# Kernel optimization log

Hardware: AMD Instinct MI355X
Metric: run time of the kernel (lower is better)

The kernel has to match this reference:

```python
import jax, jax.numpy as jnp
import numpy as np

N_M, N_D, N_A = 100000, 30000, 80000


def setup_inputs() -> dict:
    key = jax.random.key(0)
    ks = jax.random.split(key, 24)
    d_in, d_h, d_out = 64, 64, 32
    inp = {
        "x_movie": jax.random.normal(ks[0], (N_M, d_in), jnp.float32),
        "x_director": jax.random.normal(ks[1], (N_D, d_in), jnp.float32),
        "x_actor": jax.random.normal(ks[2], (N_A, d_in), jnp.float32),
        "src_md": jax.random.randint(ks[3], (1500000,), 0, N_M, jnp.int32),
        "dst_md": jax.random.randint(ks[4], (1500000,), 0, N_D, jnp.int32),
        "ew_md": jax.random.uniform(ks[5], (1500000,), jnp.float32),
        "src_dm": jax.random.randint(ks[6], (1500000,), 0, N_D, jnp.int32),
        "dst_dm": jax.random.randint(ks[7], (1500000,), 0, N_M, jnp.int32),
        "ew_dm": jax.random.uniform(ks[8], (1500000,), jnp.float32),
        "src_ma": jax.random.randint(ks[9], (2000000,), 0, N_M, jnp.int32),
        "dst_ma": jax.random.randint(ks[10], (2000000,), 0, N_A, jnp.int32),
        "ew_ma": jax.random.uniform(ks[11], (2000000,), jnp.float32),
        "src_am": jax.random.randint(ks[12], (2000000,), 0, N_A, jnp.int32),
        "dst_am": jax.random.randint(ks[13], (2000000,), 0, N_M, jnp.int32),
        "ew_am": jax.random.uniform(ks[14], (2000000,), jnp.float32),
        "W1_rel": jax.random.normal(ks[15], (4, d_in, d_h), jnp.float32) * 0.05,
        "b1": jax.random.normal(ks[16], (4, d_h), jnp.float32) * 0.05,
        "W1_root": jax.random.normal(ks[17], (4, d_in, d_h), jnp.float32) * 0.05,
        "W2_rel": jax.random.normal(ks[18], (4, d_h, d_out), jnp.float32) * 0.05,
        "b2": jax.random.normal(ks[19], (4, d_out), jnp.float32) * 0.05,
        "W2_root": jax.random.normal(ks[20], (4, d_h, d_out), jnp.float32) * 0.05,
    }
    return inp


def _hetero_layer(x_m, x_d, x_a, edges, ews, W_rel, b, W_root):
    # relation order: 0 = movie->director, 1 = director->movie,
    #                 2 = movie->actor,    3 = actor->movie
    (src_md, dst_md, src_dm, dst_dm, src_ma, dst_ma, src_am, dst_am) = edges
    (ew_md, ew_dm, ew_ma, ew_am) = ews
    # GraphConv: aggregate edge-weighted source features, then linear.
    agg_md = jax.ops.segment_sum(x_m[src_md] * ew_md[:, None], dst_md, num_segments=N_D)
    agg_dm = jax.ops.segment_sum(x_d[src_dm] * ew_dm[:, None], dst_dm, num_segments=N_M)
    agg_ma = jax.ops.segment_sum(x_m[src_ma] * ew_ma[:, None], dst_ma, num_segments=N_A)
    agg_am = jax.ops.segment_sum(x_a[src_am] * ew_am[:, None], dst_am, num_segments=N_M)
    out_d = agg_md @ W_rel[0] + b[0] + x_d @ W_root[0]
    out_m = (agg_dm @ W_rel[1] + b[1] + x_m @ W_root[1]) \
          + (agg_am @ W_rel[3] + b[3] + x_m @ W_root[3])  # HeteroConv aggr='sum'
    out_a = agg_ma @ W_rel[2] + b[2] + x_a @ W_root[2]
    return out_m, out_d, out_a


def reference(x_movie, x_director, x_actor,
              src_md, dst_md, ew_md, src_dm, dst_dm, ew_dm,
              src_ma, dst_ma, ew_ma, src_am, dst_am, ew_am,
              W1_rel, b1, W1_root, W2_rel, b2, W2_root):
    edges = (src_md, dst_md, src_dm, dst_dm, src_ma, dst_ma, src_am, dst_am)
    ews = (ew_md, ew_dm, ew_ma, ew_am)
    h_m, h_d, h_a = _hetero_layer(x_movie, x_director, x_actor, edges, ews, W1_rel, b1, W1_root)
    h_m, h_d, h_a = jax.nn.relu(h_m), jax.nn.relu(h_d), jax.nn.relu(h_a)
    o_m, o_d, o_a = _hetero_layer(h_m, h_d, h_a, edges, ews, W2_rel, b2, W2_root)
    return o_m, o_d, o_a
```

## Files before the change

### kernel.cpp

```cpp
#include <hip/hip_runtime.h>

#define N_M 100000
#define N_D 30000
#define N_A 80000

#define CSHIFT 14
#define NC_M 7
#define NC_D 2
#define NC_A 5

#define BO_MD 0
#define BO_DM (BO_MD + N_D * NC_M)
#define BO_MA (BO_DM + N_M * NC_D)
#define BO_AM (BO_MA + N_A * NC_M)
#define B_TOT (BO_AM + N_M * NC_A)

#define FBITS 12
#define NFINE 4096
#define NBUCK ((B_TOT + NFINE - 1) / NFINE)
#define T_A 4096

typedef unsigned int u32;
typedef unsigned short u16;
typedef unsigned long long u64;

__device__ __forceinline__ u16 f2bf(float f) {
  u32 u = __float_as_uint(f);
  return (u16)((u + 0x7FFFu + ((u >> 16) & 1u)) >> 16);
}
__device__ __forceinline__ float bf2f(u16 b) {
  return __uint_as_float(((u32)b) << 16);
}
__device__ __forceinline__ float bf2f_hi(u32 v) {
  return __uint_as_float(v & 0xFFFF0000u);
}
__device__ __forceinline__ u32 pack_edge(int src, float ew) {
  return ((u32)src << 15) | ((u32)f2bf(ew) & 0x7FFFu);
}
__device__ __forceinline__ float edge_w(u32 p) {
  return __uint_as_float((p & 0x7FFFu) << 16);
}

struct Rel { const int* src; const int* dst; const float* ew; int nE; int binBase; int nC; };
struct Rel4 { Rel r[4]; int blkStart[5]; };

__global__ __launch_bounds__(256) void phase0(Rel4 P, int* __restrict__ bucketHist) {
  __shared__ u32 lh[512];
  int tid = threadIdx.x;
  int b = blockIdx.x, s = 0;
  while (b >= P.blkStart[s + 1]) s++;
  const Rel R = P.r[s];
  int base = (b - P.blkStart[s]) * T_A;
  for (int i = tid; i < 512; i += 256) lh[i] = 0;
  __syncthreads();
#pragma unroll 4
  for (int k = 0; k < 16; k++) {
    int e = base + tid + k * 256;
    if (e < R.nE) {
      int key = R.binBase + R.dst[e] * R.nC + (R.src[e] >> CSHIFT);
      atomicAdd(&lh[key >> FBITS], 1u);
    }
  }
  __syncthreads();
  for (int i = tid; i < 512; i += 256) if (lh[i]) atomicAdd(&bucketHist[i], (int)lh[i]);
}

__global__ __launch_bounds__(256) void scan_bucket(const int* __restrict__ bucketHist,
                                                   int* __restrict__ bucketBase,
                                                   int* __restrict__ cursor) {
  __shared__ int wsum[4];
  int tid = threadIdx.x;
  int j0 = tid * 2;
  int a0 = (j0 < NBUCK) ? bucketHist[j0] : 0;
  int a1 = (j0 + 1 < NBUCK) ? bucketHist[j0 + 1] : 0;
  int ssum = a0 + a1;
  int lane = tid & 63, wid = tid >> 6;
  int sc = ssum;
#pragma unroll
  for (int off = 1; off < 64; off <<= 1) { int t = __shfl_up(sc, off, 64); if (lane >= off) sc += t; }
  if (lane == 63) wsum[wid] = sc;
  __syncthreads();
  int wex = 0, tot = 0;
  for (int w = 0; w < 4; w++) { int t = wsum[w]; if (w < wid) wex += t; tot += t; }
  int ex = wex + sc - ssum;
  if (j0 < NBUCK) { bucketBase[j0] = ex; cursor[j0] = ex; }
  if (j0 + 1 < NBUCK) { bucketBase[j0 + 1] = ex + a0; cursor[j0 + 1] = ex + a0; }
  if (tid == 0) bucketBase[NBUCK] = tot;
}

__global__ __launch_bounds__(256) void phaseA(Rel4 P, int* __restrict__ cursor,
                                              u64* __restrict__ tmp) {
  __shared__ u32 hist[512], lstart[512], cur[512], gbase[512];
  __shared__ u64 stage[T_A];
  __shared__ u32 wsum[4];
  int tid = threadIdx.x;
  int b = blockIdx.x, s = 0;
  while (b >= P.blkStart[s + 1]) s++;
  const Rel R = P.r[s];
  int base = (b - P.blkStart[s]) * T_A;
  int valid = min(T_A, R.nE - base);
  for (int i = tid; i < 512; i += 256) hist[i] = 0;
  __syncthreads();
#pragma unroll 4
  for (int k = 0; k < 16; k++) {
    int e = base + tid + k * 256;
    if (e < R.nE) {
      int key = R.binBase + R.dst[e] * R.nC + (R.src[e] >> CSHIFT);
      atomicAdd(&hist[key >> FBITS], 1u);
    }
  }
  __syncthreads();
  int c0 = tid * 2;
  u32 h0 = hist[c0], h1 = hist[c0 + 1];
  u32 ssum = h0 + h1;
  int lane = tid & 63, wid = tid >> 6;
  u32 sc = ssum;
#pragma unroll
  for (int off = 1; off < 64; off <<= 1) { int t = __shfl_up((int)sc, off, 64); if (lane >= off) sc += (u32)t; }
  if (lane == 63) wsum[wid] = sc;
  __syncthreads();
  u32 wex = 0;
  for (int w = 0; w < 4; w++) if (w < wid) wex += wsum[w];
  u32 ex = wex + sc - ssum;
// ... 58 lines not shown
  }
  if (c == NBUCK - 1 && tid == 0) bins[B_TOT] = s1;
  __syncthreads();
  for (int e = s0 + tid; e < s1; e += 256) {
    u64 t = tmp[e];
    u32 fine = (u32)(t >> 32) & (NFINE - 1);
    u32 pos = atomicAdd(&cur2[fine], 1u);
    pairs[s0 + pos] = (u32)t;
  }
}

__global__ __launch_bounds__(256) void l1_tr_m(
    const float* __restrict__ x,
    const float* __restrict__ Wr0, const float* __restrict__ Wr2,
    const float* __restrict__ Wt1, const float* __restrict__ Wt3,
    const float* __restrict__ b1a, const float* __restrict__ b1b,
    u16* __restrict__ t0, u16* __restrict__ t2, u16* __restrict__ r, int n) {
  __shared__ float A[4096], B[4096], C[4096];
  for (int i = threadIdx.x * 4; i < 4096; i += 1024) {
    *(float4*)&A[i] = *(const float4*)&Wr0[i];
    *(float4*)&B[i] = *(const float4*)&Wr2[i];
    float4 p = *(const float4*)&Wt1[i], q = *(const float4*)&Wt3[i];
    *(float4*)&C[i] = make_float4(p.x + q.x, p.y + q.y, p.z + q.z, p.w + q.w);
  }
  __syncthreads();
  int lane = threadIdx.x & 63, wid = threadIdx.x >> 6;
  int wave = blockIdx.x * 4 + wid, nW = gridDim.x * 4;
  float bj = b1a[lane] + b1b[lane];
  for (int base = wave * 4; base < n; base += nW * 4) {
    int n0 = base, n1 = min(base + 1, n - 1), n2 = min(base + 2, n - 1), n3 = min(base + 3, n - 1);
    float o0a = 0, o0b = 0, o0c = bj, o1a = 0, o1b = 0, o1c = bj;
    float o2a = 0, o2b = 0, o2c = bj, o3a = 0, o3b = 0, o3c = bj;
#pragma unroll 4
    for (int k = 0; k < 64; k++) {
      float wa = A[k * 64 + lane], wb = B[k * 64 + lane], wc = C[k * 64 + lane];
      float x0 = x[(size_t)n0 * 64 + k], x1 = x[(size_t)n1 * 64 + k];
      float x2 = x[(size_t)n2 * 64 + k], x3 = x[(size_t)n3 * 64 + k];
      o0a = fmaf(x0, wa, o0a); o0b = fmaf(x0, wb, o0b); o0c = fmaf(x0, wc, o0c);
      o1a = fmaf(x1, wa, o1a); o1b = fmaf(x1, wb, o1b); o1c = fmaf(x1, wc, o1c);
      o2a = fmaf(x2, wa, o2a); o2b = fmaf(x2, wb, o2b); o2c = fmaf(x2, wc, o2c);
      o3a = fmaf(x3, wa, o3a); o3b = fmaf(x3, wb, o3b); o3c = fmaf(x3, wc, o3c);
    }
    t0[(size_t)n0 * 64 + lane] = f2bf(o0a); t2[(size_t)n0 * 64 + lane] = f2bf(o0b); r[(size_t)n0 * 64 + lane] = f2bf(o0c);
    if (base + 1 < n) { t0[(size_t)n1 * 64 + lane] = f2bf(o1a); t2[(size_t)n1 * 64 + lane] = f2bf(o1b); r[(size_t)n1 * 64 + lane] = f2bf(o1c); }
    if (base + 2 < n) { t0[(size_t)n2 * 64 + lane] = f2bf(o2a); t2[(size_t)n2 * 64 + lane] = f2bf(o2b); r[(size_t)n2 * 64 + lane] = f2bf(o2c); }
    if (base + 3 < n) { t0[(size_t)n3 * 64 + lane] = f2bf(o3a); t2[(size_t)n3 * 64 + lane] = f2bf(o3b); r[(size_t)n3 * 64 + lane] = f2bf(o3c); }
  }
}

__global__ __launch_bounds__(256) void l1_tr_s(
    const float* __restrict__ x,
    const float* __restrict__ Wrel, const float* __restrict__ Wroot,
    const float* __restrict__ bias,
    u16* __restrict__ t, u16* __restrict__ r, int n) {
  __shared__ float A[4096], C[4096];
  for (int i = threadIdx.x * 4; i < 4096; i += 1024) {
    *(float4*)&A[i] = *(const float4*)&Wrel[i];
    *(float4*)&C[i] = *(const float4*)&Wroot[i];
  }
  __syncthreads();
  int lane = threadIdx.x & 63, wid = threadIdx.x >> 6;
  int wave = blockIdx.x * 4 + wid, nW = gridDim.x * 4;
  float bj = bias[lane];
  for (int base = wave * 4; base < n; base += nW * 4) {
    int n0 = base, n1 = min(base + 1, n - 1), n2 = min(base + 2, n - 1), n3 = min(base + 3, n - 1);
    float o0a = 0, o0c = bj, o1a = 0, o1c = bj, o2a = 0, o2c = bj, o3a = 0, o3c = bj;
#pragma unroll 4
    for (int k = 0; k < 64; k++) {
      float wa = A[k * 64 + lane], wc = C[k * 64 + lane];
      float x0 = x[(size_t)n0 * 64 + k], x1 = x[(size_t)n1 * 64 + k];
      float x2 = x[(size_t)n2 * 64 + k], x3 = x[(size_t)n3 * 64 + k];
      o0a = fmaf(x0, wa, o0a); o0c = fmaf(x0, wc, o0c);
      o1a = fmaf(x1, wa, o1a); o1c = fmaf(x1, wc, o1c);
      o2a = fmaf(x2, wa, o2a); o2c = fmaf(x2, wc, o2c);
      o3a = fmaf(x3, wa, o3a); o3c = fmaf(x3, wc, o3c);
    }
    t[(size_t)n0 * 64 + lane] = f2bf(o0a); r[(size_t)n0 * 64 + lane] = f2bf(o0c);
    if (base + 1 < n) { t[(size_t)n1 * 64 + lane] = f2bf(o1a); r[(size_t)n1 * 64 + lane] = f2bf(o1c); }
    if (base + 2 < n) { t[(size_t)n2 * 64 + lane] = f2bf(o2a); r[(size_t)n2 * 64 + lane] = f2bf(o2c); }
    if (base + 3 < n) { t[(size_t)n3 * 64 + lane] = f2bf(o3a); r[(size_t)n3 * 64 + lane] = f2bf(o3c); }
  }
}

__device__ __forceinline__ void gather2_seg64(
    int s0, int s1, const u32* __restrict__ pairs,
    const u16* __restrict__ tbl, int lanebyte, int half, int lane,
    float& a0, float& a1) {
  for (int base = s0; base < s1; base += 64) {
    int cnt = s1 - base; if (cnt > 64) cnt = 64;
    u32 pw = 0;
    if (base + lane < s1) pw = pairs[base + lane];
    int e = 0;
    for (; e + 4 <= cnt; e += 4) {
      u32 pa0 = __builtin_amdgcn_readlane(pw, e);
      u32 pb0 = __builtin_amdgcn_readlane(pw, e + 1);
      u32 pa1 = __builtin_amdgcn_readlane(pw, e + 2);
      u32 pb1 = __builtin_amdgcn_readlane(pw, e + 3);
      u32 off0 = (half ? ((pb0 >> 15) << 7) : ((pa0 >> 15) << 7)) + lanebyte;
      u32 off1 = (half ? ((pb1 >> 15) << 7) : ((pa1 >> 15) << 7)) + lanebyte;
      u32 v0 = *(const u32*)((const char*)tbl + off0);
      u32 v1 = *(const u32*)((const char*)tbl + off1);
      float w0 = half ? edge_w(pb0) : edge_w(pa0);
      float w1 = half ? edge_w(pb1) : edge_w(pa1);
      a0 = fmaf(w0, bf2f((u16)v0), a0);
      a1 = fmaf(w0, bf2f_hi(v0), a1);
      a0 = fmaf(w1, bf2f((u16)v1), a0);
      a1 = fmaf(w1, bf2f_hi(v1), a1);
    }
    if (e + 2 <= cnt) {
      u32 pa = __builtin_amdgcn_readlane(pw, e);
      u32 pb = __builtin_amdgcn_readlane(pw, e + 1);
      u32 off = (half ? ((pb >> 15) << 7) : ((pa >> 15) << 7)) + lanebyte;
      u32 v = *(const u32*)((const char*)tbl + off);
      float w = half ? edge_w(pb) : edge_w(pa);
      a0 = fmaf(w, bf2f((u16)v), a0);
      a1 = fmaf(w, bf2f_hi(v), a1);
      e += 2;
    }
    if (e < cnt) {
      u32 p = __builtin_amdgcn_readlane(pw, e);
      if (!half) {
        u32 off = ((p >> 15) << 7) + lanebyte;
        u32 v = *(const u32*)((const char*)tbl + off);
        float w = edge_w(p);
        a0 = fmaf(w, bf2f((u16)v), a0);
        a1 = fmaf(w, bf2f_hi(v), a1);
      }
    }
  }
}

__device__ __forceinline__ void gather4_seg32(
    int s0, int s1, const u32* __restrict__ pairs,
    const u16* __restrict__ ytbl, int lanebyte, int quart, int lane,
    float& a0, float& a1) {
  for (int base = s0; base < s1; base += 64) {
    int cnt = s1 - base; if (cnt > 64) cnt = 64;
    u32 pw = 0;
    if (base + lane < s1) pw = pairs[base + lane];
    int e = 0;
    for (; e + 4 <= cnt; e += 4) {
      u32 p0 = __builtin_amdgcn_readlane(pw, e);
      u32 p1 = __builtin_amdgcn_readlane(pw, e + 1);
      u32 p2 = __builtin_amdgcn_readlane(pw, e + 2);
      u32 p3 = __builtin_amdgcn_readlane(pw, e + 3);
      u32 o0 = (p0 >> 15) << 6, o1 = (p1 >> 15) << 6;
      u32 o2 = (p2 >> 15) << 6, o3 = (p3 >> 15) << 6;
      u32 olo = (quart & 1) ? o1 : o0;
      u32 ohi = (quart & 1) ? o3 : o2;
      u32 off = ((quart & 2) ? ohi : olo) + lanebyte;
      float wlo = (quart & 1) ? edge_w(p1) : edge_w(p0);
      float whi = (quart & 1) ? edge_w(p3) : edge_w(p2);
      float w = (quart & 2) ? whi : wlo;
      u32 v = *(const u32*)((const char*)ytbl + off);
      a0 = fmaf(w, bf2f((u16)v), a0);
      a1 = fmaf(w, bf2f_hi(v), a1);
    }
    int rem = cnt - e;
    if (rem > 0) {
      u32 p0 = __builtin_amdgcn_readlane(pw, e);
      u32 p1 = (rem > 1) ? __builtin_amdgcn_readlane(pw, e + 1) : p0;
      u32 p2 = (rem > 2) ? __builtin_amdgcn_readlane(pw, e + 2) : p0;
      u32 o0 = (p0 >> 15) << 6, o1 = (p1 >> 15) << 6, o2 = (p2 >> 15) << 6;
      u32 olo = (quart & 1) ? o1 : o0;
      u32 off = ((quart & 2) ? o2 : olo) + lanebyte;
      float wlo = (quart & 1) ? edge_w(p1) : edge_w(p0);
      float w = (quart & 2) ? edge_w(p2) : wlo;
      if (quart < rem) {
        u32 v = *(const u32*)((const char*)ytbl + off);
        a0 = fmaf(w, bf2f((u16)v), a0);
        a1 = fmaf(w, bf2f_hi(v), a1);
      }
    }
  }
}

__global__ __launch_bounds__(256) void fused1(
    const int* __restrict__ bins, const u32* __restrict__ pairs,
    const u16* __restrict__ tbl, const u16* __restrict__ r1,
    const float* __restrict__ W2r, const float* __restrict__ W2t,
    const float* __restrict__ b2s,
    u16* __restrict__ y, float* __restrict__ oroot,
    int n, int nC, int binBase) {
  __shared__ u16 Wy[2048], Wt[2048];
  __shared__ float bs[32];
  __shared__ __align__(16) float scr[4][64];
  for (int i = threadIdx.x; i < 2048; i += 256) { Wy[i] = f2bf(W2r[i]); Wt[i] = f2bf(W2t[i]); }
  if (threadIdx.x < 32) bs[threadIdx.x] = b2s[threadIdx.x];
  __syncthreads();
  int lane = threadIdx.x & 63, wid = threadIdx.x >> 6;
  int j = lane & 31, half = lane >> 5;
  int lanebyte = j << 2;
  int node0 = (blockIdx.x * 4 + wid) * 8;
  int bnd = bins[binBase + (node0 + min(lane, 8)) * nC];
  float acc0[8], acc1[8];
#pragma unroll
  for (int i = 0; i < 8; i++) { acc0[i] = 0.f; acc1[i] = 0.f; }
#pragma unroll
  for (int i = 0; i < 8; i++) {
    int s0 = __builtin_amdgcn_readlane(bnd, i);
    int s1 = __builtin_amdgcn_readlane(bnd, i + 1);
    if (node0 + i < n) gather2_seg64(s0, s1, pairs, tbl, lanebyte, half, lane, acc0[i], acc1[i]);
  }
#pragma unroll
  for (int i = 0; i < 8; i++) {
    int node = node0 + i;
    if (node >= n) continue;
    float a0 = acc0[i] + __shfl_xor(acc0[i], 32);
    float a1 = acc1[i] + __shfl_xor(acc1[i], 32);
    u32 rv = *(const u32*)&r1[(size_t)node * 64 + 2 * j];
    float hv0 = fmaxf(a0 + bf2f((u16)rv), 0.f);
    float hv1 = fmaxf(a1 + bf2f_hi(rv), 0.f);
    if (!half) *(float2*)&scr[wid][2 * j] = make_float2(hv0, hv1);
    float oy = 0.f, ot = 0.f;
#pragma unroll
    for (int kk = 0; kk < 32; kk++) {
      int k = (half << 5) + kk;
      float s = scr[wid][k];
      oy = fmaf(s, bf2f(Wy[k * 32 + j]), oy);
      ot = fmaf(s, bf2f(Wt[k * 32 + j]), ot);
    }
    oy += __shfl_xor(oy, 32);
    ot += __shfl_xor(ot, 32);
    if (lane < 32) {
      y[(size_t)node * 32 + lane] = f2bf(oy);
      oroot[(size_t)node * 32 + lane] = ot + bs[lane];
    }
  }
}

__global__ __launch_bounds__(256) void fusedm(
    const int* __restrict__ bins, const u32* __restrict__ pairs,
    const u16* __restrict__ tbl1,
    const u16* __restrict__ tbl2,
    const u16* __restrict__ r1,
    const float* __restrict__ W2r0, const float* __restrict__ W2r2,
    const float* __restrict__ W2t1, const float* __restrict__ W2t3,
    const float* __restrict__ b2a, const float* __restrict__ b2b,
    u16* __restrict__ y0, u16* __restrict__ y2, float* __restrict__ oroot, int n) {
  __shared__ u16 Wy0[2048], Wy2[2048], Wt[2048];
  __shared__ float bs[32];
  __shared__ __align__(16) float scr[4][64];
  for (int i = threadIdx.x; i < 2048; i += 256) {
    Wy0[i] = f2bf(W2r0[i]); Wy2[i] = f2bf(W2r2[i]); Wt[i] = f2bf(W2t1[i] + W2t3[i]);
  }
  if (threadIdx.x < 32) bs[threadIdx.x] = b2a[threadIdx.x] + b2b[threadIdx.x];
  __syncthreads();
  int lane = threadIdx.x & 63, wid = threadIdx.x >> 6;
  int j = lane & 31, half = lane >> 5;
  int lanebyte = j << 2;
  int node0 = (blockIdx.x * 4 + wid) * 8;
  int bdm = bins[BO_DM + (node0 + min(lane, 8)) * NC_D];
  int bam = bins[BO_AM + (node0 + min(lane, 8)) * NC_A];
  float acc0[8], acc1[8];
#pragma unroll
  for (int i = 0; i < 8; i++) { acc0[i] = 0.f; acc1[i] = 0.f; }
#pragma unroll
  for (int i = 0; i < 8; i++) {
    int s0 = __builtin_amdgcn_readlane(bdm, i);
    int s1 = __builtin_amdgcn_readlane(bdm, i + 1);
    if (node0 + i < n) gather2_seg64(s0, s1, pairs, tbl1, lanebyte, half, lane, acc0[i], acc1[i]);
  }
#pragma unroll
  for (int i = 0; i < 8; i++) {
    int s0 = __builtin_amdgcn_readlane(bam, i);
    int s1 = __builtin_amdgcn_readlane(bam, i + 1);
    if (node0 + i < n) gather2_seg64(s0, s1, pairs, tbl2, lanebyte, half, lane, acc0[i], acc1[i]);
  }
#pragma unroll
  for (int i = 0; i < 8; i++) {
    int node = node0 + i;
    if (node >= n) continue;
    float a0 = acc0[i] + __shfl_xor(acc0[i], 32);
    float a1 = acc1[i] + __shfl_xor(acc1[i], 32);
    u32 rv = *(const u32*)&r1[(size_t)node * 64 + 2 * j];
    float hv0 = fmaxf(a0 + bf2f((u16)rv), 0.f);
    float hv1 = fmaxf(a1 + bf2f_hi(rv), 0.f);
    if (!half) *(float2*)&scr[wid][2 * j] = make_float2(hv0, hv1);
    float o0 = 0.f, o2 = 0.f, ot = 0.f;
#pragma unroll
    for (int kk = 0; kk < 32; kk++) {
      int k = (half << 5) + kk;
      float s = scr[wid][k];
      o0 = fmaf(s, bf2f(Wy0[k * 32 + j]), o0);
      o2 = fmaf(s, bf2f(Wy2[k * 32 + j]), o2);
      ot = fmaf(s, bf2f(Wt[k * 32 + j]), ot);
    }
    o0 += __shfl_xor(o0, 32);
    o2 += __shfl_xor(o2, 32);
    ot += __shfl_xor(ot, 32);
    if (lane < 32) {
      y0[(size_t)node * 32 + lane] = f2bf(o0);
      y2[(size_t)node * 32 + lane] = f2bf(o2);
      oroot[(size_t)node * 32 + lane] = ot + bs[lane];
    }
  }
}

__global__ __launch_bounds__(256) void out1(
    const int* __restrict__ bins, const u32* __restrict__ pairs,
    const u16* __restrict__ ytbl, float* __restrict__ out,
    int n, int nC, int binBase) {
  int lane = threadIdx.x & 63, wid = threadIdx.x >> 6;
  int node0 = (blockIdx.x * 4 + wid) * 8;
  int j = lane & 15, quart = lane >> 4;
  int lanebyte = j << 2;
  int bnd = bins[binBase + (node0 + min(lane, 8)) * nC];
  float acc0[8], acc1[8];
#pragma unroll
  for (int i = 0; i < 8; i++) { acc0[i] = 0.f; acc1[i] = 0.f; }
#pragma unroll
  for (int i = 0; i < 8; i++) {
    int s0 = __builtin_amdgcn_readlane(bnd, i);
    int s1 = __builtin_amdgcn_readlane(bnd, i + 1);
    if (node0 + i < n) gather4_seg32(s0, s1, pairs, ytbl, lanebyte, quart, lane, acc0[i], acc1[i]);
  }
#pragma unroll
  for (int i = 0; i < 8; i++) {
    int node = node0 + i;
    if (node >= n) continue;
    float a0 = acc0[i] + __shfl_xor(acc0[i], 16);
    a0 += __shfl_xor(a0, 32);
    float a1 = acc1[i] + __shfl_xor(acc1[i], 16);
    a1 += __shfl_xor(a1, 32);
    if (lane < 16) {
      float2* o = (float2*)&out[(size_t)node * 32 + 2 * j];
      float2 v = *o;
      v.x += a0; v.y += a1;
      *o = v;
    }
  }
}

__global__ __launch_bounds__(256) void outm(
    const int* __restrict__ bins, const u32* __restrict__ pairs,
    const u16* __restrict__ y1,
    const u16* __restrict__ y2,
    float* __restrict__ out, int n) {
  int lane = threadIdx.x & 63, wid = threadIdx.x >> 6;
  int node0 = (blockIdx.x * 4 + wid) * 8;
  int j = lane & 15, quart = lane >> 4;
  int lanebyte = j << 2;
  int bdm = bins[BO_DM + (node0 + min(lane, 8)) * NC_D];
  int bam = bins[BO_AM + (node0 + min(lane, 8)) * NC_A];
  float acc0[8], acc1[8];
#pragma unroll
  for (int i = 0; i < 8; i++) { acc0[i] = 0.f; acc1[i] = 0.f; }
#pragma unroll
  for (int i = 0; i < 8; i++) {
    int s0 = __builtin_amdgcn_readlane(bdm, i);
    int s1 = __builtin_amdgcn_readlane(bdm, i + 1);
    if (node0 + i < n) gather4_seg32(s0, s1, pairs, y1, lanebyte, quart, lane, acc0[i], acc1[i]);
  }
#pragma unroll
  for (int i = 0; i < 8; i++) {
    int s0 = __builtin_amdgcn_readlane(bam, i);
    int s1 = __builtin_amdgcn_readlane(bam, i + 1);
    if (node0 + i < n) gather4_seg32(s0, s1, pairs, y2, lanebyte, quart, lane, acc0[i], acc1[i]);
  }
#pragma unroll
  for (int i = 0; i < 8; i++) {
    int node = node0 + i;
    if (node >= n) continue;
    float a0 = acc0[i] + __shfl_xor(acc0[i], 16);
    a0 += __shfl_xor(a0, 32);
    float a1 = acc1[i] + __shfl_xor(acc1[i], 16);
    a1 += __shfl_xor(a1, 32);
    if (lane < 16) {
      float2* o = (float2*)&out[(size_t)node * 32 + 2 * j];
      float2 v = *o;
      v.x += a0; v.y += a1;
      *o = v;
    }
  }
}

static inline int nblkA(long long e) { return (int)((e + T_A - 1) / T_A); }

extern "C" void kernel_launch(void* const* d_in, const int* in_sizes, int n_in,
                              void* d_out, int out_size, void* d_ws, size_t ws_size,
                              hipStream_t stream) {
  const float* x_m = (const float*)d_in[0];
  const float* x_d = (const float*)d_in[1];
  const float* x_a = (const float*)d_in[2];
  const int* src_md = (const int*)d_in[3];
  const int* dst_md = (const int*)d_in[4];
  const float* ew_md = (const float*)d_in[5];
  const int* src_dm = (const int*)d_in[6];
  const int* dst_dm = (const int*)d_in[7];
  const float* ew_dm = (const float*)d_in[8];
  const int* src_ma = (const int*)d_in[9];
  const int* dst_ma = (const int*)d_in[10];
  const float* ew_ma = (const float*)d_in[11];
  const int* src_am = (const int*)d_in[12];
  const int* dst_am = (const int*)d_in[13];
  const float* ew_am = (const float*)d_in[14];
  const float* W1_rel = (const float*)d_in[15];
  const float* b1 = (const float*)d_in[16];
  const float* W1_root = (const float*)d_in[17];
  const float* W2_rel = (const float*)d_in[18];
  const float* b2 = (const float*)d_in[19];
  const float* W2_root = (const float*)d_in[20];

  const int E_md = in_sizes[3];
  const int E_dm = in_sizes[6];
  const int E_ma = in_sizes[9];
  const int E_am = in_sizes[12];
  const long long E_tot = (long long)E_md + E_dm + E_ma + E_am;

  char* w = (char*)d_ws;
  u64* tmp = (u64*)w;       w += (size_t)E_tot * 8;
  u32* pairs = (u32*)w;     w += (size_t)E_tot * 4;
  int* bins = (int*)w;      w += (size_t)(B_TOT + 1) * 4;
  int* bucketHist = (int*)w; w += 512 * 4;
  int* bucketBase = (int*)w; w += (NBUCK + 1) * 4;
  int* cursor = (int*)w;     w += 512 * 4;
  u16* r_d  = (u16*)w;      w += (size_t)N_D * 64 * 2;
  u16* r_a  = (u16*)w;      w += (size_t)N_A * 64 * 2;
  u16* y_md = (u16*)w;      w += (size_t)N_M * 32 * 2;
  u16* y_dm = (u16*)w;      w += (size_t)N_D * 32 * 2;
  u16* y_ma = (u16*)w;      w += (size_t)N_M * 32 * 2;
  u16* y_am = (u16*)w;      w += (size_t)N_A * 32 * 2;
  if ((size_t)(w - (char*)d_ws) > ws_size) return;
  char* ta = (char*)tmp;
  u16* t_md = (u16*)ta;     ta += (size_t)N_M * 64 * 2;
  u16* t_dm = (u16*)ta;     ta += (size_t)N_D * 64 * 2;
  u16* t_ma = (u16*)ta;     ta += (size_t)N_M * 64 * 2;
  u16* t_am = (u16*)ta;     ta += (size_t)N_A * 64 * 2;
  u16* r_m  = (u16*)ta;     ta += (size_t)N_M * 64 * 2;

  float* o_m = (float*)d_out;
  float* o_d = o_m + (size_t)N_M * 32;
  float* o_a = o_d + (size_t)N_D * 32;

  hipMemsetAsync(bucketHist, 0, 512 * 4, stream);

  Rel4 P;
  P.r[0] = { src_md, dst_md, ew_md, E_md, BO_MD, NC_M };
  P.r[1] = { src_dm, dst_dm, ew_dm, E_dm, BO_DM, NC_D };
  P.r[2] = { src_ma, dst_ma, ew_ma, E_ma, BO_MA, NC_M };
  P.r[3] = { src_am, dst_am, ew_am, E_am, BO_AM, NC_A };
  P.blkStart[0] = 0;
  P.blkStart[1] = P.blkStart[0] + nblkA(E_md);
  P.blkStart[2] = P.blkStart[1] + nblkA(E_dm);
  P.blkStart[3] = P.blkStart[2] + nblkA(E_ma);
  P.blkStart[4] = P.blkStart[3] + nblkA(E_am);

  phase0<<<P.blkStart[4], 256, 0, stream>>>(P, bucketHist);
  scan_bucket<<<1, 256, 0, stream>>>(bucketHist, bucketBase, cursor);
  phaseA<<<P.blkStart[4], 256, 0, stream>>>(P, cursor, tmp);
  phaseB<<<NBUCK, 256, 0, stream>>>(tmp, bucketBase, pairs, bins);

  l1_tr_m<<<768, 256, 0, stream>>>(x_m, W1_rel + 0 * 4096, W1_rel + 2 * 4096,
                                   W1_root + 1 * 4096, W1_root + 3 * 4096,
                                   b1 + 1 * 64, b1 + 3 * 64, t_md, t_ma, r_m, N_M);
  l1_tr_s<<<512, 256, 0, stream>>>(x_d, W1_rel + 1 * 4096, W1_root + 0 * 4096,
                                   b1 + 0 * 64, t_dm, r_d, N_D);
  l1_tr_s<<<512, 256, 0, stream>>>(x_a, W1_rel + 3 * 4096, W1_root + 2 * 4096,
                                   b1 + 2 * 64, t_am, r_a, N_A);

  fused1<<<(N_D + 31) / 32, 256, 0, stream>>>(bins, pairs, t_md, r_d,
      W2_rel + 1 * 2048, W2_root + 0 * 2048, b2 + 0 * 32, y_dm, o_d, N_D, NC_M, BO_MD);
  fused1<<<(N_A + 31) / 32, 256, 0, stream>>>(bins, pairs, t_ma, r_a,
      W2_rel + 3 * 2048, W2_root + 2 * 2048, b2 + 2 * 32, y_am, o_a, N_A, NC_M, BO_MA);
  fusedm<<<(N_M + 31) / 32, 256, 0, stream>>>(bins, pairs, t_dm, t_am, r_m,
      W2_rel + 0 * 2048, W2_rel + 2 * 2048, W2_root + 1 * 2048, W2_root + 3 * 2048,
      b2 + 1 * 32, b2 + 3 * 32, y_md, y_ma, o_m, N_M);

  out1<<<(N_D + 31) / 32, 256, 0, stream>>>(bins, pairs, y_md, o_d, N_D, NC_M, BO_MD);
  out1<<<(N_A + 31) / 32, 256, 0, stream>>>(bins, pairs, y_ma, o_a, N_A, NC_M, BO_MA);
  outm<<<(N_M + 31) / 32, 256, 0, stream>>>(bins, pairs, y_dm, y_am, o_m, N_M);
}
```

Measured before the change: 1.042 ms.

## Widen gather loads to 8 bytes and distribute edges via ds_bpermute

The gather loops in the fused and output kernels are rewritten. Each lane now loads 8 bytes (four bf16 features) per edge instead of 4 bytes. A wave handles 4 edges per step for the 64-wide tables and 8 edges per step for the 32-wide tables, with each lane group picking its edge via ds_bpermute instead of readlane and select chains. The aim is fewer load instructions and less scalar selection per edge. The cost is twice as many accumulators, extra shuffle-reduction steps, and padded tail iterations that rely on zeroed pair words producing zero weights.

```diff
diff --git a/kernel.cpp b/kernel.cpp
--- a/kernel.cpp
+++ b/kernel.cpp
@@ -36,9 +36,6 @@
 }
 __device__ __forceinline__ u32 pack_edge(int src, float ew) {
   return ((u32)src << 15) | ((u32)f2bf(ew) & 0x7FFFu);
-}
-__device__ __forceinline__ float edge_w(u32 p) {
-  return __uint_as_float((p & 0x7FFFu) << 16);
 }
 
 struct Rel { const int* src; const int* dst; const float* ew; int nE; int binBase; int nC; };
@@ -263,95 +260,49 @@
   }
 }
 
-__device__ __forceinline__ void gather2_seg64(
+
+__device__ __forceinline__ void gatherq_64(
     int s0, int s1, const u32* __restrict__ pairs,
-    const u16* __restrict__ tbl, int lanebyte, int half, int lane,
-    float& a0, float& a1) {
+    const u16* __restrict__ tbl, int lanebyte, int qaddr, int lane,
+    float& a0, float& a1, float& a2, float& a3) {
   for (int base = s0; base < s1; base += 64) {
-    int cnt = s1 - base; if (cnt > 64) cnt = 64;
     u32 pw = 0;
     if (base + lane < s1) pw = pairs[base + lane];
-    int e = 0;
-    for (; e + 4 <= cnt; e += 4) {
-      u32 pa0 = __builtin_amdgcn_readlane(pw, e);
-      u32 pb0 = __builtin_amdgcn_readlane(pw, e + 1);
-      u32 pa1 = __builtin_amdgcn_readlane(pw, e + 2);
-      u32 pb1 = __builtin_amdgcn_readlane(pw, e + 3);
-      u32 off0 = (half ? ((pb0 >> 15) << 7) : ((pa0 >> 15) << 7)) + lanebyte;
-      u32 off1 = (half ? ((pb1 >> 15) << 7) : ((pa1 >> 15) << 7)) + lanebyte;
-      u32 v0 = *(const u32*)((const char*)tbl + off0);
-      u32 v1 = *(const u32*)((const char*)tbl + off1);
-      float w0 = half ? edge_w(pb0) : edge_w(pa0);
-      float w1 = half ? edge_w(pb1) : edge_w(pa1);
-      a0 = fmaf(w0, bf2f((u16)v0), a0);
-      a1 = fmaf(w0, bf2f_hi(v0), a1);
-      a0 = fmaf(w1, bf2f((u16)v1), a0);
-      a1 = fmaf(w1, bf2f_hi(v1), a1);
-    }
-    if (e + 2 <= cnt) {
-      u32 pa = __builtin_amdgcn_readlane(pw, e);
-      u32 pb = __builtin_amdgcn_readlane(pw, e + 1);
-      u32 off = (half ? ((pb >> 15) << 7) : ((pa >> 15) << 7)) + lanebyte;
-      u32 v = *(const u32*)((const char*)tbl + off);
-      float w = half ? edge_w(pb) : edge_w(pa);
-      a0 = fmaf(w, bf2f((u16)v), a0);
-      a1 = fmaf(w, bf2f_hi(v), a1);
-      e += 2;
-    }
-    if (e < cnt) {
-      u32 p = __builtin_amdgcn_readlane(pw, e);
-      if (!half) {
-        u32 off = ((p >> 15) << 7) + lanebyte;
-        u32 v = *(const u32*)((const char*)tbl + off);
-        float w = edge_w(p);
-        a0 = fmaf(w, bf2f((u16)v), a0);
-        a1 = fmaf(w, bf2f_hi(v), a1);
-      }
-    }
-  }
-}
-
-__device__ __forceinline__ void gather4_seg32(
+    int ng = min(s1 - base, 64);
+    ng = (ng + 3) >> 2;
+#pragma unroll 2
+    for (int g = 0; g < ng; g++) {
+      u32 p = (u32)__builtin_amdgcn_ds_bpermute(qaddr + (g << 4), (int)pw);
+      u32 off = ((p >> 15) << 7) + lanebyte;
+      float w = __uint_as_float((p & 0x7FFFu) << 16);
+      uint2 v = *(const uint2*)((const char*)tbl + off);
+      a0 = fmaf(w, bf2f((u16)v.x), a0);
+      a1 = fmaf(w, bf2f_hi(v.x), a1);
+      a2 = fmaf(w, bf2f((u16)v.y), a2);
+      a3 = fmaf(w, bf2f_hi(v.y), a3);
+    }
+  }
+}
+
+__device__ __forceinline__ void gathero_32(
     int s0, int s1, const u32* __restrict__ pairs,
-    const u16* __restrict__ ytbl, int lanebyte, int quart, int lane,
-    float& a0, float& a1) {
+    const u16* __restrict__ ytbl, int lanebyte, int oaddr, int lane,
+    float& a0, float& a1, float& a2, float& a3) {
   for (int base = s0; base < s1; base += 64) {
-    int cnt = s1 - base; if (cnt > 64) cnt = 64;
     u32 pw = 0;
     if (base + lane < s1) pw = pairs[base + lane];
-    int e = 0;
-    for (; e + 4 <= cnt; e += 4) {
-      u32 p0 = __builtin_amdgcn_readlane(pw, e);
-      u32 p1 = __builtin_amdgcn_readlane(pw, e + 1);
-      u32 p2 = __builtin_amdgcn_readlane(pw, e + 2);
-      u32 p3 = __builtin_amdgcn_readlane(pw, e + 3);
-      u32 o0 = (p0 >> 15) << 6, o1 = (p1 >> 15) << 6;
-      u32 o2 = (p2 >> 15) << 6, o3 = (p3 >> 15) << 6;
-      u32 olo = (quart & 1) ? o1 : o0;
-      u32 ohi = (quart & 1) ? o3 : o2;
-      u32 off = ((quart & 2) ? ohi : olo) + lanebyte;
-      float wlo = (quart & 1) ? edge_w(p1) : edge_w(p0);
-      float whi = (quart & 1) ? edge_w(p3) : edge_w(p2);
-      float w = (quart & 2) ? whi : wlo;
-      u32 v = *(const u32*)((const char*)ytbl + off);
-      a0 = fmaf(w, bf2f((u16)v), a0);
-      a1 = fmaf(w, bf2f_hi(v), a1);
-    }
-    int rem = cnt - e;
-    if (rem > 0) {
-      u32 p0 = __builtin_amdgcn_readlane(pw, e);
-      u32 p1 = (rem > 1) ? __builtin_amdgcn_readlane(pw, e + 1) : p0;
-      u32 p2 = (rem > 2) ? __builtin_amdgcn_readlane(pw, e + 2) : p0;
-      u32 o0 = (p0 >> 15) << 6, o1 = (p1 >> 15) << 6, o2 = (p2 >> 15) << 6;
-      u32 olo = (quart & 1) ? o1 : o0;
-      u32 off = ((quart & 2) ? o2 : olo) + lanebyte;
-      float wlo = (quart & 1) ? edge_w(p1) : edge_w(p0);
-      float w = (quart & 2) ? edge_w(p2) : wlo;
-      if (quart < rem) {
-        u32 v = *(const u32*)((const char*)ytbl + off);
-        a0 = fmaf(w, bf2f((u16)v), a0);
-        a1 = fmaf(w, bf2f_hi(v), a1);
-      }
+    int ng = min(s1 - base, 64);
+    ng = (ng + 7) >> 3;
+#pragma unroll 2
+    for (int g = 0; g < ng; g++) {
+      u32 p = (u32)__builtin_amdgcn_ds_bpermute(oaddr + (g << 5), (int)pw);
+      u32 off = ((p >> 15) << 6) + lanebyte;
+      float w = __uint_as_float((p & 0x7FFFu) << 16);
+      uint2 v = *(const uint2*)((const char*)ytbl + off);
+      a0 = fmaf(w, bf2f((u16)v.x), a0);
+      a1 = fmaf(w, bf2f_hi(v.x), a1);
+      a2 = fmaf(w, bf2f((u16)v.y), a2);
+      a3 = fmaf(w, bf2f_hi(v.y), a3);
     }
   }
 }
@@ -371,28 +322,36 @@
   __syncthreads();
   int lane = threadIdx.x & 63, wid = threadIdx.x >> 6;
   int j = lane & 31, half = lane >> 5;
-  int lanebyte = j << 2;
+  int j4 = lane & 15, quart = lane >> 4;
+  int lanebyte = j4 << 3;
+  int qaddr = quart << 2;
   int node0 = (blockIdx.x * 4 + wid) * 8;
   int bnd = bins[binBase + (node0 + min(lane, 8)) * nC];
-  float acc0[8], acc1[8];
-#pragma unroll
-  for (int i = 0; i < 8; i++) { acc0[i] = 0.f; acc1[i] = 0.f; }
+  float acc0[8], acc1[8], acc2[8], acc3[8];
+#pragma unroll
+  for (int i = 0; i < 8; i++) { acc0[i] = 0.f; acc1[i] = 0.f; acc2[i] = 0.f; acc3[i] = 0.f; }
 #pragma unroll
   for (int i = 0; i < 8; i++) {
     int s0 = __builtin_amdgcn_readlane(bnd, i);
     int s1 = __builtin_amdgcn_readlane(bnd, i + 1);
-    if (node0 + i < n) gather2_seg64(s0, s1, pairs, tbl, lanebyte, half, lane, acc0[i], acc1[i]);
+    if (node0 + i < n) gatherq_64(s0, s1, pairs, tbl, lanebyte, qaddr, lane,
+                                  acc0[i], acc1[i], acc2[i], acc3[i]);
   }
 #pragma unroll
   for (int i = 0; i < 8; i++) {
     int node = node0 + i;
     if (node >= n) continue;
-    float a0 = acc0[i] + __shfl_xor(acc0[i], 32);
-    float a1 = acc1[i] + __shfl_xor(acc1[i], 32);
-    u32 rv = *(const u32*)&r1[(size_t)node * 64 + 2 * j];
-    float hv0 = fmaxf(a0 + bf2f((u16)rv), 0.f);
-    float hv1 = fmaxf(a1 + bf2f_hi(rv), 0.f);
-    if (!half) *(float2*)&scr[wid][2 * j] = make_float2(hv0, hv1);
+    float a0 = acc0[i], a1 = acc1[i], a2 = acc2[i], a3 = acc3[i];
+    a0 += __shfl_xor(a0, 16); a0 += __shfl_xor(a0, 32);
+    a1 += __shfl_xor(a1, 16); a1 += __shfl_xor(a1, 32);
+    a2 += __shfl_xor(a2, 16); a2 += __shfl_xor(a2, 32);
+    a3 += __shfl_xor(a3, 16); a3 += __shfl_xor(a3, 32);
+    uint2 rv = *(const uint2*)((const char*)r1 + (size_t)node * 128 + lanebyte);
+    float hv0 = fmaxf(a0 + bf2f((u16)rv.x), 0.f);
+    float hv1 = fmaxf(a1 + bf2f_hi(rv.x), 0.f);
+    float hv2 = fmaxf(a2 + bf2f((u16)rv.y), 0.f);
+    float hv3 = fmaxf(a3 + bf2f_hi(rv.y), 0.f);
+    if (quart == 0) *(float4*)&scr[wid][4 * j4] = make_float4(hv0, hv1, hv2, hv3);
     float oy = 0.f, ot = 0.f;
 #pragma unroll
     for (int kk = 0; kk < 32; kk++) {
@@ -429,35 +388,44 @@
   __syncthreads();
   int lane = threadIdx.x & 63, wid = threadIdx.x >> 6;
   int j = lane & 31, half = lane >> 5;
-  int lanebyte = j << 2;
+  int j4 = lane & 15, quart = lane >> 4;
+  int lanebyte = j4 << 3;
+  int qaddr = quart << 2;
   int node0 = (blockIdx.x * 4 + wid) * 8;
   int bdm = bins[BO_DM + (node0 + min(lane, 8)) * NC_D];
   int bam = bins[BO_AM + (node0 + min(lane, 8)) * NC_A];
-  float acc0[8], acc1[8];
-#pragma unroll
-  for (int i = 0; i < 8; i++) { acc0[i] = 0.f; acc1[i] = 0.f; }
+  float acc0[8], acc1[8], acc2[8], acc3[8];
+#pragma unroll
+  for (int i = 0; i < 8; i++) { acc0[i] = 0.f; acc1[i] = 0.f; acc2[i] = 0.f; acc3[i] = 0.f; }
 #pragma unroll
   for (int i = 0; i < 8; i++) {
     int s0 = __builtin_amdgcn_readlane(bdm, i);
     int s1 = __builtin_amdgcn_readlane(bdm, i + 1);
-    if (node0 + i < n) gather2_seg64(s0, s1, pairs, tbl1, lanebyte, half, lane, acc0[i], acc1[i]);
+    if (node0 + i < n) gatherq_64(s0, s1, pairs, tbl1, lanebyte, qaddr, lane,
+                                  acc0[i], acc1[i], acc2[i], acc3[i]);
   }
 #pragma unroll
   for (int i = 0; i < 8; i++) {
     int s0 = __builtin_amdgcn_readlane(bam, i);
     int s1 = __builtin_amdgcn_readlane(bam, i + 1);
-    if (node0 + i < n) gather2_seg64(s0, s1, pairs, tbl2, lanebyte, half, lane, acc0[i], acc1[i]);
+    if (node0 + i < n) gatherq_64(s0, s1, pairs, tbl2, lanebyte, qaddr, lane,
+                                  acc0[i], acc1[i], acc2[i], acc3[i]);
   }
 #pragma unroll
   for (int i = 0; i < 8; i++) {
     int node = node0 + i;
     if (node >= n) continue;
-    float a0 = acc0[i] + __shfl_xor(acc0[i], 32);
-    float a1 = acc1[i] + __shfl_xor(acc1[i], 32);
-    u32 rv = *(const u32*)&r1[(size_t)node * 64 + 2 * j];
-    float hv0 = fmaxf(a0 + bf2f((u16)rv), 0.f);
-    float hv1 = fmaxf(a1 + bf2f_hi(rv), 0.f);
-    if (!half) *(float2*)&scr[wid][2 * j] = make_float2(hv0, hv1);
+    float a0 = acc0[i], a1 = acc1[i], a2 = acc2[i], a3 = acc3[i];
+    a0 += __shfl_xor(a0, 16); a0 += __shfl_xor(a0, 32);
+    a1 += __shfl_xor(a1, 16); a1 += __shfl_xor(a1, 32);
+    a2 += __shfl_xor(a2, 16); a2 += __shfl_xor(a2, 32);
+    a3 += __shfl_xor(a3, 16); a3 += __shfl_xor(a3, 32);
+    uint2 rv = *(const uint2*)((const char*)r1 + (size_t)node * 128 + lanebyte);
+    float hv0 = fmaxf(a0 + bf2f((u16)rv.x), 0.f);
+    float hv1 = fmaxf(a1 + bf2f_hi(rv.x), 0.f);
+    float hv2 = fmaxf(a2 + bf2f((u16)rv.y), 0.f);
+    float hv3 = fmaxf(a3 + bf2f_hi(rv.y), 0.f);
+    if (quart == 0) *(float4*)&scr[wid][4 * j4] = make_float4(hv0, hv1, hv2, hv3);
     float o0 = 0.f, o2 = 0.f, ot = 0.f;
 #pragma unroll
     for (int kk = 0; kk < 32; kk++) {
@@ -484,30 +452,33 @@
     int n, int nC, int binBase) {
   int lane = threadIdx.x & 63, wid = threadIdx.x >> 6;
   int node0 = (blockIdx.x * 4 + wid) * 8;
-  int j = lane & 15, quart = lane >> 4;
-  int lanebyte = j << 2;
+  int j8 = lane & 7;
+  int lanebyte = j8 << 3;
+  int oaddr = (lane >> 3) << 2;
   int bnd = bins[binBase + (node0 + min(lane, 8)) * nC];
-  float acc0[8], acc1[8];
-#pragma unroll
-  for (int i = 0; i < 8; i++) { acc0[i] = 0.f; acc1[i] = 0.f; }
+  float acc0[8], acc1[8], acc2[8], acc3[8];
+#pragma unroll
+  for (int i = 0; i < 8; i++) { acc0[i] = 0.f; acc1[i] = 0.f; acc2[i] = 0.f; acc3[i] = 0.f; }
 #pragma unroll
   for (int i = 0; i < 8; i++) {
     int s0 = __builtin_amdgcn_readlane(bnd, i);
     int s1 = __builtin_amdgcn_readlane(bnd, i + 1);
-    if (node0 + i < n) gather4_seg32(s0, s1, pairs, ytbl, lanebyte, quart, lane, acc0[i], acc1[i]);
+    if (node0 + i < n) gathero_32(s0, s1, pairs, ytbl, lanebyte, oaddr, lane,
+                                  acc0[i], acc1[i], acc2[i], acc3[i]);
   }
 #pragma unroll
   for (int i = 0; i < 8; i++) {
     int node = node0 + i;
     if (node >= n) continue;
-    float a0 = acc0[i] + __shfl_xor(acc0[i], 16);
-    a0 += __shfl_xor(a0, 32);
-    float a1 = acc1[i] + __shfl_xor(acc1[i], 16);
-    a1 += __shfl_xor(a1, 32);
-    if (lane < 16) {
-      float2* o = (float2*)&out[(size_t)node * 32 + 2 * j];
-      float2 v = *o;
-      v.x += a0; v.y += a1;
+    float a0 = acc0[i], a1 = acc1[i], a2 = acc2[i], a3 = acc3[i];
+    a0 += __shfl_xor(a0, 8); a0 += __shfl_xor(a0, 16); a0 += __shfl_xor(a0, 32);
+    a1 += __shfl_xor(a1, 8); a1 += __shfl_xor(a1, 16); a1 += __shfl_xor(a1, 32);
+    a2 += __shfl_xor(a2, 8); a2 += __shfl_xor(a2, 16); a2 += __shfl_xor(a2, 32);
+    a3 += __shfl_xor(a3, 8); a3 += __shfl_xor(a3, 16); a3 += __shfl_xor(a3, 32);
+    if (lane < 8) {
+      float4* o = (float4*)((char*)out + (size_t)node * 128 + (j8 << 4));
+      float4 v = *o;
+      v.x += a0; v.y += a1; v.z += a2; v.w += a3;
       *o = v;
     }
   }
@@ -520,37 +491,41 @@
     float* __restrict__ out, int n) {
   int lane = threadIdx.x & 63, wid = threadIdx.x >> 6;
   int node0 = (blockIdx.x * 4 + wid) * 8;
-  int j = lane & 15, quart = lane >> 4;
-  int lanebyte = j << 2;
+  int j8 = lane & 7;
+  int lanebyte = j8 << 3;
+  int oaddr = (lane >> 3) << 2;
   int bdm = bins[BO_DM + (node0 + min(lane, 8)) * NC_D];
   int bam = bins[BO_AM + (node0 + min(lane, 8)) * NC_A];
-  float acc0[8], acc1[8];
-#pragma unroll
-  for (int i = 0; i < 8; i++) { acc0[i] = 0.f; acc1[i] = 0.f; }
+  float acc0[8], acc1[8], acc2[8], acc3[8];
+#pragma unroll
+  for (int i = 0; i < 8; i++) { acc0[i] = 0.f; acc1[i] = 0.f; acc2[i] = 0.f; acc3[i] = 0.f; }
 #pragma unroll
   for (int i = 0; i < 8; i++) {
     int s0 = __builtin_amdgcn_readlane(bdm, i);
     int s1 = __builtin_amdgcn_readlane(bdm, i + 1);
-    if (node0 + i < n) gather4_seg32(s0, s1, pairs, y1, lanebyte, quart, lane, acc0[i], acc1[i]);
+    if (node0 + i < n) gathero_32(s0, s1, pairs, y1, lanebyte, oaddr, lane,
+                                  acc0[i], acc1[i], acc2[i], acc3[i]);
   }
 #pragma unroll
   for (int i = 0; i < 8; i++) {
     int s0 = __builtin_amdgcn_readlane(bam, i);
     int s1 = __builtin_amdgcn_readlane(bam, i + 1);
-    if (node0 + i < n) gather4_seg32(s0, s1, pairs, y2, lanebyte, quart, lane, acc0[i], acc1[i]);
+    if (node0 + i < n) gathero_32(s0, s1, pairs, y2, lanebyte, oaddr, lane,
+                                  acc0[i], acc1[i], acc2[i], acc3[i]);
   }
 #pragma unroll
   for (int i = 0; i < 8; i++) {
     int node = node0 + i;
     if (node >= n) continue;
-    float a0 = acc0[i] + __shfl_xor(acc0[i], 16);
-    a0 += __shfl_xor(a0, 32);
-    float a1 = acc1[i] + __shfl_xor(acc1[i], 16);
-    a1 += __shfl_xor(a1, 32);
-    if (lane < 16) {
-      float2* o = (float2*)&out[(size_t)node * 32 + 2 * j];
-      float2 v = *o;
-      v.x += a0; v.y += a1;
+    float a0 = acc0[i], a1 = acc1[i], a2 = acc2[i], a3 = acc3[i];
+    a0 += __shfl_xor(a0, 8); a0 += __shfl_xor(a0, 16); a0 += __shfl_xor(a0, 32);
+    a1 += __shfl_xor(a1, 8); a1 += __shfl_xor(a1, 16); a1 += __shfl_xor(a1, 32);
+    a2 += __shfl_xor(a2, 8); a2 += __shfl_xor(a2, 16); a2 += __shfl_xor(a2, 32);
+    a3 += __shfl_xor(a3, 8); a3 += __shfl_xor(a3, 16); a3 += __shfl_xor(a3, 32);
+    if (lane < 8) {
+      float4* o = (float4*)((char*)out + (size_t)node * 128 + (j8 << 4));
+      float4 v = *o;
+      v.x += a0; v.y += a1; v.z += a2; v.w += a3;
       *o = v;
     }
   }
```

Result: no change. 1.027 ms (-1.4%).

## Gather layer-2 edges 8-at-a-time with bpermute and 8-byte loads; 512-thread fused blocks

Applied to the files above, without the earlier changes.

The layer-2 output gather now maps eight lanes per edge, so each wave processes eight edges per iteration. Each lane loads 8 bytes (four bf16 values), and the edge word is distributed with ds_bpermute instead of readlane chains plus selects. Reductions use three xor shuffles and float4 read-modify-write stores. Separately, the fused layer-1 kernels move to 512-thread blocks covering 64 nodes each, which amortizes the per-block shared-memory weight conversion over more nodes but may reduce occupancy.

```diff
diff --git a/kernel.cpp b/kernel.cpp
--- a/kernel.cpp
+++ b/kernel.cpp
@@ -311,52 +311,30 @@
   }
 }
 
-__device__ __forceinline__ void gather4_seg32(
+__device__ __forceinline__ void gathero_32(
     int s0, int s1, const u32* __restrict__ pairs,
-    const u16* __restrict__ ytbl, int lanebyte, int quart, int lane,
-    float& a0, float& a1) {
+    const u16* __restrict__ ytbl, int lanebyte, int oaddr, int lane,
+    float& a0, float& a1, float& a2, float& a3) {
   for (int base = s0; base < s1; base += 64) {
-    int cnt = s1 - base; if (cnt > 64) cnt = 64;
     u32 pw = 0;
     if (base + lane < s1) pw = pairs[base + lane];
-    int e = 0;
-    for (; e + 4 <= cnt; e += 4) {
-      u32 p0 = __builtin_amdgcn_readlane(pw, e);
-      u32 p1 = __builtin_amdgcn_readlane(pw, e + 1);
-      u32 p2 = __builtin_amdgcn_readlane(pw, e + 2);
-      u32 p3 = __builtin_amdgcn_readlane(pw, e + 3);
-      u32 o0 = (p0 >> 15) << 6, o1 = (p1 >> 15) << 6;
-      u32 o2 = (p2 >> 15) << 6, o3 = (p3 >> 15) << 6;
-      u32 olo = (quart & 1) ? o1 : o0;
-      u32 ohi = (quart & 1) ? o3 : o2;
-      u32 off = ((quart & 2) ? ohi : olo) + lanebyte;
-      float wlo = (quart & 1) ? edge_w(p1) : edge_w(p0);
-      float whi = (quart & 1) ? edge_w(p3) : edge_w(p2);
-      float w = (quart & 2) ? whi : wlo;
-      u32 v = *(const u32*)((const char*)ytbl + off);
-      a0 = fmaf(w, bf2f((u16)v), a0);
-      a1 = fmaf(w, bf2f_hi(v), a1);
-    }
-    int rem = cnt - e;
-    if (rem > 0) {
-      u32 p0 = __builtin_amdgcn_readlane(pw, e);
-      u32 p1 = (rem > 1) ? __builtin_amdgcn_readlane(pw, e + 1) : p0;
-      u32 p2 = (rem > 2) ? __builtin_amdgcn_readlane(pw, e + 2) : p0;
-      u32 o0 = (p0 >> 15) << 6, o1 = (p1 >> 15) << 6, o2 = (p2 >> 15) << 6;
-      u32 olo = (quart & 1) ? o1 : o0;
-      u32 off = ((quart & 2) ? o2 : olo) + lanebyte;
-      float wlo = (quart & 1) ? edge_w(p1) : edge_w(p0);
-      float w = (quart & 2) ? edge_w(p2) : wlo;
-      if (quart < rem) {
-        u32 v = *(const u32*)((const char*)ytbl + off);
-        a0 = fmaf(w, bf2f((u16)v), a0);
-        a1 = fmaf(w, bf2f_hi(v), a1);
-      }
-    }
-  }
-}
-
-__global__ __launch_bounds__(256) void fused1(
+    int ng = min(s1 - base, 64);
+    ng = (ng + 7) >> 3;
+#pragma unroll 2
+    for (int g = 0; g < ng; g++) {
+      u32 p = (u32)__builtin_amdgcn_ds_bpermute(oaddr + (g << 5), (int)pw);
+      u32 off = ((p >> 15) << 6) + lanebyte;
+      float w = __uint_as_float((p & 0x7FFFu) << 16);
+      uint2 v = *(const uint2*)((const char*)ytbl + off);
+      a0 = fmaf(w, bf2f((u16)v.x), a0);
+      a1 = fmaf(w, bf2f_hi(v.x), a1);
+      a2 = fmaf(w, bf2f((u16)v.y), a2);
+      a3 = fmaf(w, bf2f_hi(v.y), a3);
+    }
+  }
+}
+
+__global__ __launch_bounds__(512) void fused1(
     const int* __restrict__ bins, const u32* __restrict__ pairs,
     const u16* __restrict__ tbl, const u16* __restrict__ r1,
     const float* __restrict__ W2r, const float* __restrict__ W2t,
@@ -365,14 +343,14 @@
     int n, int nC, int binBase) {
   __shared__ u16 Wy[2048], Wt[2048];
   __shared__ float bs[32];
-  __shared__ __align__(16) float scr[4][64];
-  for (int i = threadIdx.x; i < 2048; i += 256) { Wy[i] = f2bf(W2r[i]); Wt[i] = f2bf(W2t[i]); }
+  __shared__ __align__(16) float scr[8][64];
+  for (int i = threadIdx.x; i < 2048; i += 512) { Wy[i] = f2bf(W2r[i]); Wt[i] = f2bf(W2t[i]); }
   if (threadIdx.x < 32) bs[threadIdx.x] = b2s[threadIdx.x];
   __syncthreads();
   int lane = threadIdx.x & 63, wid = threadIdx.x >> 6;
   int j = lane & 31, half = lane >> 5;
   int lanebyte = j << 2;
-  int node0 = (blockIdx.x * 4 + wid) * 8;
+  int node0 = (blockIdx.x * 8 + wid) * 8;
   int bnd = bins[binBase + (node0 + min(lane, 8)) * nC];
   float acc0[8], acc1[8];
 #pragma unroll
@@ -410,7 +388,7 @@
   }
 }
 
-__global__ __launch_bounds__(256) void fusedm(
+__global__ __launch_bounds__(512) void fusedm(
     const int* __restrict__ bins, const u32* __restrict__ pairs,
     const u16* __restrict__ tbl1,
     const u16* __restrict__ tbl2,
@@ -421,8 +399,8 @@
     u16* __restrict__ y0, u16* __restrict__ y2, float* __restrict__ oroot, int n) {
   __shared__ u16 Wy0[2048], Wy2[2048], Wt[2048];
   __shared__ float bs[32];
-  __shared__ __align__(16) float scr[4][64];
-  for (int i = threadIdx.x; i < 2048; i += 256) {
+  __shared__ __align__(16) float scr[8][64];
+  for (int i = threadIdx.x; i < 2048; i += 512) {
     Wy0[i] = f2bf(W2r0[i]); Wy2[i] = f2bf(W2r2[i]); Wt[i] = f2bf(W2t1[i] + W2t3[i]);
   }
   if (threadIdx.x < 32) bs[threadIdx.x] = b2a[threadIdx.x] + b2b[threadIdx.x];
@@ -430,7 +408,7 @@
   int lane = threadIdx.x & 63, wid = threadIdx.x >> 6;
   int j = lane & 31, half = lane >> 5;
   int lanebyte = j << 2;
-  int node0 = (blockIdx.x * 4 + wid) * 8;
+  int node0 = (blockIdx.x * 8 + wid) * 8;
   int bdm = bins[BO_DM + (node0 + min(lane, 8)) * NC_D];
   int bam = bins[BO_AM + (node0 + min(lane, 8)) * NC_A];
   float acc0[8], acc1[8];
@@ -484,30 +462,33 @@
     int n, int nC, int binBase) {
   int lane = threadIdx.x & 63, wid = threadIdx.x >> 6;
   int node0 = (blockIdx.x * 4 + wid) * 8;
-  int j = lane & 15, quart = lane >> 4;
-  int lanebyte = j << 2;
+  int j8 = lane & 7;
+  int lanebyte = j8 << 3;
+  int oaddr = (lane >> 3) << 2;
   int bnd = bins[binBase + (node0 + min(lane, 8)) * nC];
-  float acc0[8], acc1[8];
-#pragma unroll
-  for (int i = 0; i < 8; i++) { acc0[i] = 0.f; acc1[i] = 0.f; }
+  float acc0[8], acc1[8], acc2[8], acc3[8];
+#pragma unroll
+  for (int i = 0; i < 8; i++) { acc0[i] = 0.f; acc1[i] = 0.f; acc2[i] = 0.f; acc3[i] = 0.f; }
 #pragma unroll
   for (int i = 0; i < 8; i++) {
     int s0 = __builtin_amdgcn_readlane(bnd, i);
     int s1 = __builtin_amdgcn_readlane(bnd, i + 1);
-    if (node0 + i < n) gather4_seg32(s0, s1, pairs, ytbl, lanebyte, quart, lane, acc0[i], acc1[i]);
+    if (node0 + i < n) gathero_32(s0, s1, pairs, ytbl, lanebyte, oaddr, lane,
+                                  acc0[i], acc1[i], acc2[i], acc3[i]);
   }
 #pragma unroll
   for (int i = 0; i < 8; i++) {
     int node = node0 + i;
     if (node >= n) continue;
-    float a0 = acc0[i] + __shfl_xor(acc0[i], 16);
-    a0 += __shfl_xor(a0, 32);
-    float a1 = acc1[i] + __shfl_xor(acc1[i], 16);
-    a1 += __shfl_xor(a1, 32);
-    if (lane < 16) {
-      float2* o = (float2*)&out[(size_t)node * 32 + 2 * j];
-      float2 v = *o;
-      v.x += a0; v.y += a1;
+    float a0 = acc0[i], a1 = acc1[i], a2 = acc2[i], a3 = acc3[i];
+    a0 += __shfl_xor(a0, 8); a0 += __shfl_xor(a0, 16); a0 += __shfl_xor(a0, 32);
+    a1 += __shfl_xor(a1, 8); a1 += __shfl_xor(a1, 16); a1 += __shfl_xor(a1, 32);
+    a2 += __shfl_xor(a2, 8); a2 += __shfl_xor(a2, 16); a2 += __shfl_xor(a2, 32);
+    a3 += __shfl_xor(a3, 8); a3 += __shfl_xor(a3, 16); a3 += __shfl_xor(a3, 32);
+    if (lane < 8) {
+      float4* o = (float4*)((char*)out + (size_t)node * 128 + (j8 << 4));
+      float4 v = *o;
+      v.x += a0; v.y += a1; v.z += a2; v.w += a3;
       *o = v;
     }
   }
@@ -520,37 +501,41 @@
     float* __restrict__ out, int n) {
   int lane = threadIdx.x & 63, wid = threadIdx.x >> 6;
   int node0 = (blockIdx.x * 4 + wid) * 8;
-  int j = lane & 15, quart = lane >> 4;
-  int lanebyte = j << 2;
+  int j8 = lane & 7;
+  int lanebyte = j8 << 3;
+  int oaddr = (lane >> 3) << 2;
   int bdm = bins[BO_DM + (node0 + min(lane, 8)) * NC_D];
   int bam = bins[BO_AM + (node0 + min(lane, 8)) * NC_A];
-  float acc0[8], acc1[8];
-#pragma unroll
-  for (int i = 0; i < 8; i++) { acc0[i] = 0.f; acc1[i] = 0.f; }
+  float acc0[8], acc1[8], acc2[8], acc3[8];
+#pragma unroll
+  for (int i = 0; i < 8; i++) { acc0[i] = 0.f; acc1[i] = 0.f; acc2[i] = 0.f; acc3[i] = 0.f; }
 #pragma unroll
   for (int i = 0; i < 8; i++) {
     int s0 = __builtin_amdgcn_readlane(bdm, i);
     int s1 = __builtin_amdgcn_readlane(bdm, i + 1);
-    if (node0 + i < n) gather4_seg32(s0, s1, pairs, y1, lanebyte, quart, lane, acc0[i], acc1[i]);
+    if (node0 + i < n) gathero_32(s0, s1, pairs, y1, lanebyte, oaddr, lane,
+                                  acc0[i], acc1[i], acc2[i], acc3[i]);
   }
 #pragma unroll
   for (int i = 0; i < 8; i++) {
     int s0 = __builtin_amdgcn_readlane(bam, i);
     int s1 = __builtin_amdgcn_readlane(bam, i + 1);
-    if (node0 + i < n) gather4_seg32(s0, s1, pairs, y2, lanebyte, quart, lane, acc0[i], acc1[i]);
+    if (node0 + i < n) gathero_32(s0, s1, pairs, y2, lanebyte, oaddr, lane,
+                                  acc0[i], acc1[i], acc2[i], acc3[i]);
   }
 #pragma unroll
   for (int i = 0; i < 8; i++) {
     int node = node0 + i;
     if (node >= n) continue;
-    float a0 = acc0[i] + __shfl_xor(acc0[i], 16);
-    a0 += __shfl_xor(a0, 32);
-    float a1 = acc1[i] + __shfl_xor(acc1[i], 16);
-    a1 += __shfl_xor(a1, 32);
-    if (lane < 16) {
-      float2* o = (float2*)&out[(size_t)node * 32 + 2 * j];
-      float2 v = *o;
-      v.x += a0; v.y += a1;
+    float a0 = acc0[i], a1 = acc1[i], a2 = acc2[i], a3 = acc3[i];
+    a0 += __shfl_xor(a0, 8); a0 += __shfl_xor(a0, 16); a0 += __shfl_xor(a0, 32);
+    a1 += __shfl_xor(a1, 8); a1 += __shfl_xor(a1, 16); a1 += __shfl_xor(a1, 32);
+    a2 += __shfl_xor(a2, 8); a2 += __shfl_xor(a2, 16); a2 += __shfl_xor(a2, 32);
+    a3 += __shfl_xor(a3, 8); a3 += __shfl_xor(a3, 16); a3 += __shfl_xor(a3, 32);
+    if (lane < 8) {
+      float4* o = (float4*)((char*)out + (size_t)node * 128 + (j8 << 4));
+      float4 v = *o;
+      v.x += a0; v.y += a1; v.z += a2; v.w += a3;
       *o = v;
     }
   }
@@ -640,11 +625,11 @@
   l1_tr_s<<<512, 256, 0, stream>>>(x_a, W1_rel + 3 * 4096, W1_root + 2 * 4096,
                                    b1 + 2 * 64, t_am, r_a, N_A);
 
-  fused1<<<(N_D + 31) / 32, 256, 0, stream>>>(bins, pairs, t_md, r_d,
+  fused1<<<(N_D + 63) / 64, 512, 0, stream>>>(bins, pairs, t_md, r_d,
       W2_rel + 1 * 2048, W2_root + 0 * 2048, b2 + 0 * 32, y_dm, o_d, N_D, NC_M, BO_MD);
-  fused1<<<(N_A + 31) / 32, 256, 0, stream>>>(bins, pairs, t_ma, r_a,
+  fused1<<<(N_A + 63) / 64, 512, 0, stream>>>(bins, pairs, t_ma, r_a,
       W2_rel + 3 * 2048, W2_root + 2 * 2048, b2 + 2 * 32, y_am, o_a, N_A, NC_M, BO_MA);
-  fusedm<<<(N_M + 31) / 32, 256, 0, stream>>>(bins, pairs, t_dm, t_am, r_m,
+  fusedm<<<(N_M + 63) / 64, 512, 0, stream>>>(bins, pairs, t_dm, t_am, r_m,
       W2_rel + 0 * 2048, W2_rel + 2 * 2048, W2_root + 1 * 2048, W2_root + 3 * 2048,
       b2 + 1 * 32, b2 + 3 * 32, y_md, y_ma, o_m, N_M);
 
```

After: 989.7 us. -5.0%, faster.
